# Kernel tuning notes

Hardware: AMD Instinct MI355X
Metric: run time of the kernel (lower is better)

The kernel has to match this reference:

```python
import jax, jax.numpy as jnp
import numpy as np
import math

N, IN, OUT, E, K = 50000, 256, 256, 800000, 32

def setup_inputs() -> dict:
    key = jax.random.key(0)
    k0, k1, k2, k3, k4 = jax.random.split(key, 5)
    feat = jax.random.normal(k0, (N, IN), dtype=jnp.float32)
    # xavier_uniform with relu gain, as in reset_parameters
    gain = math.sqrt(2.0)
    a = gain * math.sqrt(6.0 / (IN + OUT))
    W_self = jax.random.uniform(k1, (OUT, IN), minval=-a, maxval=a, dtype=jnp.float32)
    W_neigh = jax.random.uniform(k2, (OUT, IN), minval=-a, maxval=a, dtype=jnp.float32)
    b_neigh = jnp.zeros((OUT,), dtype=jnp.float32)
    # random CSR graph: E edges, row pointers from sorted cut points
    indices = jax.random.randint(k3, (E,), 0, N, dtype=jnp.int32)
    inner = jnp.sort(jax.random.randint(k4, (N - 1,), 0, E, dtype=jnp.int32))
    indptr = jnp.concatenate([jnp.zeros((1,), jnp.int32), inner,
                              jnp.full((1,), E, jnp.int32)])
    return {"feat": feat, "W_self": W_self, "W_neigh": W_neigh,
            "b_neigh": b_neigh, "indices": indices, "indptr": indptr}

def reference(feat, W_self, W_neigh, b_neigh, indices, indptr):
    n = feat.shape[0]
    # feat_drop with p=0.0 is identity
    h_self = feat @ W_self.T                      # [N, OUT]
    feat_neigh = feat @ W_neigh.T + b_neigh       # [N, OUT]
    # MaxK: keep top-k entries per row, zero the rest
    vals, idx = jax.lax.top_k(feat_neigh, K)      # [N, K]
    rows = jnp.arange(n)[:, None]
    masked = jnp.zeros_like(feat_neigh).at[rows, idx].set(vals)
    # CSR SpMM with unit values (sum over neighbors)
    deg = indptr[1:] - indptr[:-1]                # [N]
    dst = jnp.repeat(jnp.arange(n, dtype=jnp.int32), deg,
                     total_repeat_length=indices.shape[0])
    h_neigh = jax.ops.segment_sum(masked[indices], dst, num_segments=n)
    return h_self + h_neigh
```

## Files before the change

### kernel.cpp

```cpp
#include <hip/hip_runtime.h>

#define N_NODES 50000
#define TOPK 32
#define SOFT_DELTA 2e-5f

typedef unsigned long long u64;
typedef unsigned u32;
typedef float f32x16 __attribute__((ext_vector_type(16)));
typedef __bf16 bf16x8 __attribute__((ext_vector_type(8)));

__device__ __forceinline__ float dec(u32 u) {
    return __builtin_bit_cast(float, (u & 0x80000000u) ? (u & 0x7FFFFFFFu) : ~u);
}
__device__ __forceinline__ int mbcnt64(u64 m) {
    return __builtin_amdgcn_mbcnt_hi((u32)(m >> 32),
           __builtin_amdgcn_mbcnt_lo((u32)m, 0u));
}

__device__ __forceinline__ void gll16(const uint4* g, uint4* l) {
    __builtin_amdgcn_global_load_lds(
        (const __attribute__((address_space(1))) void*)g,
        (__attribute__((address_space(3))) void*)l, 16, 0, 0);
}

__device__ __forceinline__ u32 enc4(float v, int col) {
    return ((u32)col << 16) |
           ((__builtin_bit_cast(u32, v) + 0x8000u) >> 16);
}

__device__ __forceinline__ u32 s2(float x0, float x1, float& r0, float& r1) {
    const u32 h0 = (__builtin_bit_cast(u32, x0) + 0x8000u) & 0xFFFF0000u;
    const u32 h1 = (__builtin_bit_cast(u32, x1) + 0x8000u) & 0xFFFF0000u;
    r0 = x0 - __builtin_bit_cast(float, h0);
    r1 = x1 - __builtin_bit_cast(float, h1);
    return (h0 >> 16) | h1;
}
__device__ __forceinline__ u32 p2(float x0, float x1) {
    return (((__builtin_bit_cast(u32, x0) + 0x8000u) & 0xFFFF0000u) >> 16) |
           ((__builtin_bit_cast(u32, x1) + 0x8000u) & 0xFFFF0000u);
}

struct Tri { uint4 h1, h2, h3; };
__device__ __forceinline__ Tri cvt8(const float4 u, const float4 v, bool deep) {
    Tri t;
    float r0,r1,r2,r3,r4,r5,r6,r7;
    t.h1.x = s2(u.x, u.y, r0, r1);
    t.h1.y = s2(u.z, u.w, r2, r3);
    t.h1.z = s2(v.x, v.y, r4, r5);
    t.h1.w = s2(v.z, v.w, r6, r7);
    float s0,s1,s2_,s3,s4,s5,s6,s7;
    t.h2.x = s2(r0, r1, s0, s1);
    t.h2.y = s2(r2, r3, s2_, s3);
    t.h2.z = s2(r4, r5, s4, s5);
    t.h2.w = s2(r6, r7, s6, s7);
    if (deep) {
        t.h3.x = p2(s0, s1); t.h3.y = p2(s2_, s3);
        t.h3.z = p2(s4, s5); t.h3.w = p2(s6, s7);
    } else {
        t.h3 = make_uint4(0, 0, 0, 0);
    }
    return t;
}

__global__ __launch_bounds__(256) void wprep_kernel(
    const float* __restrict__ Wneigh,
    uint4* __restrict__ WT1, uint4* __restrict__ WT2, uint4* __restrict__ WT3)
{
    for (int it = 0; it < 4; ++it) {
        const int id = (blockIdx.x * 4 + it) * 256 + threadIdx.x;
        const int s = id >> 10, rem = id & 1023;
        const int c = rem >> 8, j = rem & 255;
        const float* src = Wneigh + (size_t)j * 256 + s * 32 + c * 8;
        const Tri t = cvt8(*(const float4*)src, *(const float4*)(src + 4), true);
        WT1[id] = t.h1; WT2[id] = t.h2; WT3[id] = t.h3;
    }
}

__global__ __launch_bounds__(256, 2) void gemm_self_kernel(
    const float* __restrict__ feat,
    const float* __restrict__ Wself,
    float* __restrict__ hself)
{
    __shared__ uint4 LA1[512], LA2[512];
    __shared__ uint4 LB1[512], LB2[512];

    const int tid  = threadIdx.x;
    const int lane = tid & 63;
    const int wave = tid >> 6;
    const int wm   = wave >> 1;
    const int wn   = wave & 1;
    const int kg   = lane >> 5;

    const int rowTile = blockIdx.x >> 1;
    const int colTile = blockIdx.x & 1;
    const int row0 = rowTile * 128;
    const int jbase = colTile << 7;

    const int srow  = tid >> 1;
    const int shalf = tid & 1;
    int gra = row0 + srow;
    if (gra >= N_NODES) gra = 0;
    const float* pa = feat  + (size_t)gra * 256 + shalf * 16;
    const float* pb = Wself + (size_t)(jbase + srow) * 256 + shalf * 16;
    const int i0 = ((shalf * 2) << 7) + srow;
    const int i1 = i0 + 128;

    const int rA0 = wm * 64 + (lane & 31);
    const int rB0 = wn * 64 + (lane & 31);

    f32x16 acc[2][2];
#pragma unroll
    for (int i = 0; i < 2; ++i)
#pragma unroll
        for (int j = 0; j < 2; ++j) acc[i][j] = (f32x16)0.f;

    float4 va0, va1, va2, va3, vb0, vb1, vb2, vb3;
    va0 = *(const float4*)(pa);      va1 = *(const float4*)(pa + 4);
    va2 = *(const float4*)(pa + 8);  va3 = *(const float4*)(pa + 12);
    vb0 = *(const float4*)(pb);      vb1 = *(const float4*)(pb + 4);
    vb2 = *(const float4*)(pb + 8);  vb3 = *(const float4*)(pb + 12);

    for (int s = 0; s < 8; ++s) {
        __syncthreads();
        {
            const Tri tA0 = cvt8(va0, va1, false);
            const Tri tA1 = cvt8(va2, va3, false);
            const Tri tB0 = cvt8(vb0, vb1, false);
            const Tri tB1 = cvt8(vb2, vb3, false);
            LA1[i0] = tA0.h1; LA2[i0] = tA0.h2;
            LA1[i1] = tA1.h1; LA2[i1] = tA1.h2;
            LB1[i0] = tB0.h1; LB2[i0] = tB0.h2;
            LB1[i1] = tB1.h1; LB2[i1] = tB1.h2;
        }
        __syncthreads();

        if (s < 7) {
            const int ko = (s + 1) * 32;
            va0 = *(const float4*)(pa + ko);      va1 = *(const float4*)(pa + ko + 4);
            va2 = *(const float4*)(pa + ko + 8);  va3 = *(const float4*)(pa + ko + 12);
            vb0 = *(const float4*)(pb + ko);      vb1 = *(const float4*)(pb + ko + 4);
            vb2 = *(const float4*)(pb + ko + 8);  vb3 = *(const float4*)(pb + ko + 12);
        }

#pragma unroll
        for (int ks = 0; ks < 2; ++ks) {
            const int base = ((ks << 1) | kg) << 7;
            bf16x8 a1[2], a2[2], b1[2], b2[2];
#pragma unroll
            for (int f = 0; f < 2; ++f) {
                const int ia = base + rA0 + f * 32;
                const int ib = base + rB0 + f * 32;
                a1[f] = __builtin_bit_cast(bf16x8, LA1[ia]);
                a2[f] = __builtin_bit_cast(bf16x8, LA2[ia]);
                b1[f] = __builtin_bit_cast(bf16x8, LB1[ib]);
                b2[f] = __builtin_bit_cast(bf16x8, LB2[ib]);
            }
#pragma unroll
            for (int i = 0; i < 2; ++i)
#pragma unroll
                for (int j = 0; j < 2; ++j) {
                    acc[i][j] = __builtin_amdgcn_mfma_f32_32x32x16_bf16(
                        a1[i], b1[j], acc[i][j], 0, 0, 0);
                    acc[i][j] = __builtin_amdgcn_mfma_f32_32x32x16_bf16(
                        a1[i], b2[j], acc[i][j], 0, 0, 0);
                    acc[i][j] = __builtin_amdgcn_mfma_f32_32x32x16_bf16(
                        a2[i], b1[j], acc[i][j], 0, 0, 0);
                }
        }
    }

#pragma unroll
    for (int i = 0; i < 2; ++i) {
        const int rbase = row0 + wm * 64 + i * 32 + (kg << 2);
#pragma unroll
        for (int j = 0; j < 2; ++j) {
            const int cg = (colTile << 7) + wn * 64 + j * 32 + (lane & 31);
#pragma unroll
            for (int r = 0; r < 16; ++r) {
                const int grow = rbase + (r & 3) + ((r >> 2) << 3);
                if (grow < N_NODES)
                    hself[(size_t)grow * 256 + cg] = acc[i][j][r];
            }
        }
    }
}

__global__ __launch_bounds__(512, 4) void gemm_nt_kernel(
    const float* __restrict__ feat,
    const uint4* __restrict__ WT1, const uint4* __restrict__ WT2,
    const uint4* __restrict__ WT3,
    const float* __restrict__ bneigh,
    u32*  __restrict__ compact,
    u64*  __restrict__ softList)
{
    __shared__ uint4 SMEM[4096];
    uint4* LA1 = SMEM;
    uint4* LA2 = SMEM + 256;
    uint4* LA3 = SMEM + 512;
    uint4* LB1 = SMEM + 768;
    uint4* LB2 = SMEM + 1792;
    uint4* LB3 = SMEM + 2816;
    float* stage = (float*)SMEM;

    const int tid  = threadIdx.x;
    const int lane = tid & 63;
    const int wave = tid >> 6;
    const int kg   = lane >> 5;

    const int row0 = blockIdx.x * 64;

    const int ar = tid & 63;
    const int ac = (tid >> 6) & 3;
    int gra = row0 + ar;
    if (gra >= N_NODES) gra = row0;
    const float* pa = feat + (size_t)gra * 256 + ac * 8;
    const int aidx = ac * 64 + ar;

    const int rA0  = lane & 31;
    const int bcol = wave * 32 + (lane & 31);

    f32x16 acc[2];
    acc[0] = (f32x16)0.f; acc[1] = (f32x16)0.f;

    float4 va0 = make_float4(0,0,0,0), va1 = make_float4(0,0,0,0);
    if (tid < 256) { va0 = *(const float4*)(pa); va1 = *(const float4*)(pa + 4); }

    for (int s = 0; s < 8; ++s) {
        __syncthreads();
        {
            const int base = s * 1024;
            const int w64  = wave * 64;
            gll16(WT1 + base + w64 + lane,       LB1 + w64);
            gll16(WT1 + base + 512 + w64 + lane, LB1 + 512 + w64);
            gll16(WT2 + base + w64 + lane,       LB2 + w64);
            gll16(WT2 + base + 512 + w64 + lane, LB2 + 512 + w64);
            gll16(WT3 + base + w64 + lane,       LB3 + w64);
            gll16(WT3 + base + 512 + w64 + lane, LB3 + 512 + w64);
        }
        if (tid < 256) {
            const Tri t = cvt8(va0, va1, true);
            LA1[aidx] = t.h1; LA2[aidx] = t.h2; LA3[aidx] = t.h3;
            if (s < 7) {
                const int ko = (s + 1) * 32;
                va0 = *(const float4*)(pa + ko);
                va1 = *(const float4*)(pa + ko + 4);
            }
        }
        __syncthreads();

#pragma unroll
        for (int ks = 0; ks < 2; ++ks) {
            const int ch = (ks << 1) | kg;
            bf16x8 a1[2], a2[2], a3[2], b1, b2, b3;
            {
                const int ib = ch * 256 + bcol;
                b1 = __builtin_bit_cast(bf16x8, LB1[ib]);
                b2 = __builtin_bit_cast(bf16x8, LB2[ib]);
                b3 = __builtin_bit_cast(bf16x8, LB3[ib]);
            }
#pragma unroll
            for (int f = 0; f < 2; ++f) {
                const int ia = ch * 64 + rA0 + f * 32;
                a1[f] = __builtin_bit_cast(bf16x8, LA1[ia]);
                a2[f] = __builtin_bit_cast(bf16x8, LA2[ia]);
                a3[f] = __builtin_bit_cast(bf16x8, LA3[ia]);
            }
#pragma unroll
            for (int i = 0; i < 2; ++i) {
                acc[i] = __builtin_amdgcn_mfma_f32_32x32x16_bf16(a1[i], b1, acc[i], 0, 0, 0);
                acc[i] = __builtin_amdgcn_mfma_f32_32x32x16_bf16(a1[i], b2, acc[i], 0, 0, 0);
                acc[i] = __builtin_amdgcn_mfma_f32_32x32x16_bf16(a2[i], b1, acc[i], 0, 0, 0);
                acc[i] = __builtin_amdgcn_mfma_f32_32x32x16_bf16(a2[i], b2, acc[i], 0, 0, 0);
                acc[i] = __builtin_amdgcn_mfma_f32_32x32x16_bf16(a1[i], b3, acc[i], 0, 0, 0);
                acc[i] = __builtin_amdgcn_mfma_f32_32x32x16_bf16(a3[i], b1, acc[i], 0, 0, 0);
            }
        }
    }

    __syncthreads();
    const float bn = bneigh[bcol];
#pragma unroll
    for (int i = 0; i < 2; ++i) {
        const int rbase = i * 32 + (kg << 2);
#pragma unroll
        for (int r = 0; r < 16; ++r) {
            const int rl = rbase + (r & 3) + ((r >> 2) << 3);
            stage[rl * 256 + bcol] = acc[i][r] + bn;
        }
    }
    __syncthreads();

    for (int it = 0; it < 8; ++it) {
        const int rl  = wave * 8 + it;
        const int row = row0 + rl;
        if (row >= N_NODES) break;

        const float4 v4 = ((const float4*)stage)[rl * 64 + lane];
        const float vv[4] = {v4.x, v4.y, v4.z, v4.w};
        u32 key[4];
#pragma unroll
        for (int j = 0; j < 4; ++j) {
            const u32 b = __builtin_bit_cast(u32, vv[j]);
            key[j] = (b & 0x80000000u) ? ~b : (b | 0x80000000u);
        }

        u32 T = 0;
        bool resolved = false;
        for (int b = 31; b >= 0; --b) {
            const u32 t2 = T | (1u << b);
            int cnt = 0;
#pragma unroll
            for (int j = 0; j < 4; ++j) cnt += __popcll(__ballot(key[j] >= t2));
            if (cnt >= TOPK) T = t2;
            if (cnt == TOPK) { resolved = true; break; }
        }
        if (resolved) {
            u32 x = 0xFFFFFFFFu;
#pragma unroll
            for (int j = 0; j < 4; ++j)
                x = min(x, (key[j] >= T) ? key[j] : 0xFFFFFFFFu);
#pragma unroll
            for (int off = 32; off >= 1; off >>= 1)
                x = min(x, (u32)__shfl_xor((int)x, off, 64));
            T = x;
        }

        u64 bgt[4], beq[4];
        int cgt = 0, ceq = 0;
#pragma unroll
        for (int j = 0; j < 4; ++j) {
            bgt[j] = __ballot(key[j] > T);
            beq[j] = __ballot(key[j] == T);
            cgt += __popcll(bgt[j]);
            ceq += __popcll(beq[j]);
        }
        const int r_ = TOPK - cgt;

        u32 m33;
        if (ceq > r_) {
            m33 = T;
        } else {
            u32 x = 0;
#pragma unroll
            for (int j = 0; j < 4; ++j) x = max(x, (key[j] < T) ? key[j] : 0u);
#pragma unroll
            for (int off = 32; off >= 1; off >>= 1)
                x = max(x, (u32)__shfl_xor((int)x, off, 64));
            m33 = x;
        }
        const float v32f = dec(T);
        const float v33f = dec(m33);
        const bool soft = (v32f - v33f) < SOFT_DELTA;

        const int meqsum = mbcnt64(beq[0]) + mbcnt64(beq[1]) +
                           mbcnt64(beq[2]) + mbcnt64(beq[3]);

        int gtbase = 0, selfpre = 0, spillcol = -1;
#pragma unroll
        for (int j = 0; j < 4; ++j) {
            const int col = lane * 4 + j;
            if (key[j] > T) {
                const int pos = gtbase + mbcnt64(bgt[j]);
                compact[(size_t)row * 32 + pos] = enc4(vv[j], col);
            } else if (key[j] == T) {
                const int eqrank = meqsum + selfpre;
                if (eqrank < r_) {
                    const float w = (soft && eqrank == r_ - 1) ? 0.5f : 1.0f;
                    compact[(size_t)row * 32 + (cgt + eqrank)] = enc4(vv[j] * w, col);
                } else if (eqrank == r_) {
                    spillcol = col;
                }
                ++selfpre;
            }
            gtbase += __popcll(bgt[j]);
        }

        if (soft) {
            const u64 valbits = (u64)__builtin_bit_cast(u32, 0.5f * v33f);
            if (ceq > r_) {
                if (spillcol >= 0)
                    softList[row] = (((u64)(u32)spillcol) << 32) | valbits;
            } else {
                int best = 1 << 30;
#pragma unroll
                for (int j = 0; j < 4; ++j) {
                    const u64 b33 = __ballot(key[j] == m33);
                    if (b33) best = min(best, ((int)__builtin_ctzll(b33)) * 4 + j);
                }
                if (lane == 0)
                    softList[row] = (((u64)(u32)best) << 32) | valbits;
            }
        } else if (lane == 0) {
            softList[row] = 0ull;
        }
    }
}

__global__ __launch_bounds__(512) void spmm_kernel(
    const u32* __restrict__ compact,
    const u64* __restrict__ softList,
    const int* __restrict__ indices,
    const int* __restrict__ indptr,
    float* __restrict__ inout)
{
    __shared__ float accs[8][2][256];

    const int lane = threadIdx.x & 63;
    const int wave = threadIdx.x >> 6;
    const int node = blockIdx.x * 8 + wave;
    const int half = lane >> 5;
    const int e    = lane & 31;
    float* acc  = accs[wave][half];

    const float4 z4 = make_float4(0.f, 0.f, 0.f, 0.f);
    ((float4*)&accs[wave][0][0])[lane] = z4;
    ((float4*)&accs[wave][1][0])[lane] = z4;

    const int start = indptr[node];
    const int deg   = indptr[node + 1] - start;
    const float4 hs = ((const float4*)(inout + (size_t)node * 256))[lane];

    for (int base = 0; base < deg; base += 64) {
        const int n = min(64, deg - base);
        const int myidx = (base + lane < deg) ? indices[start + base + lane] : 0;
        for (int d = 0; d < n; d += 16) {
            int s[8]; bool ok[8]; u32 ent[8];
#pragma unroll
            for (int k = 0; k < 8; ++k) {
                const int ei = d + 2 * k + half;
                ok[k] = ei < n;
                s[k]  = __shfl(myidx, min(ei, n - 1), 64);
                ent[k] = compact[(size_t)s[k] * 32 + e];
            }
            u64 se[8];
            if (e == 0) {
#pragma unroll
                for (int k = 0; k < 8; ++k) se[k] = softList[s[k]];
            }
#pragma unroll
            for (int k = 0; k < 8; ++k) {
                const int c = (int)(ent[k] >> 16);
                float v = __builtin_bit_cast(float, ent[k] << 16);
                if (!ok[k]) v = 0.f;
                acc[c] += v;
                if (e == 0 && ok[k]) {
                    const u32 vb = (u32)se[k];
                    if (vb)
                        acc[(int)(se[k] >> 32)] += __builtin_bit_cast(float, vb);
                }
            }
        }
    }

    const float4 a0 = ((const float4*)&accs[wave][0][0])[lane];
    const float4 a1 = ((const float4*)&accs[wave][1][0])[lane];
    float4 o;
    o.x = a0.x + a1.x + hs.x;
    o.y = a0.y + a1.y + hs.y;
    o.z = a0.z + a1.z + hs.z;
    o.w = a0.w + a1.w + hs.w;
    ((float4*)(inout + (size_t)node * 256))[lane] = o;
}

extern "C" void kernel_launch(void* const* d_in, const int* in_sizes, int n_in,
                              void* d_out, int out_size, void* d_ws, size_t ws_size,
                              hipStream_t stream) {
    const float* feat   = (const float*)d_in[0];
    const float* Wself  = (const float*)d_in[1];
    const float* Wneigh = (const float*)d_in[2];
    const float* bneigh = (const float*)d_in[3];
    const int* indices  = (const int*)d_in[4];
    const int* indptr   = (const int*)d_in[5];
    float* out = (float*)d_out;

    char* ws       = (char*)d_ws;
    u32*  compact  = (u32*)(ws);
    u64*  softList = (u64*)(ws + 6400000);
    uint4* WT1     = (uint4*)(ws + 6800000);
    uint4* WT2     = WT1 + 8192;
    uint4* WT3     = WT2 + 8192;

    wprep_kernel<<<dim3(8), dim3(256), 0, stream>>>(Wneigh, WT1, WT2, WT3);

    const int rowTiles128 = (N_NODES + 127) / 128;
    gemm_self_kernel<<<dim3(rowTiles128 * 2), dim3(256), 0, stream>>>(
        feat, Wself, out);

    const int rowTiles64 = (N_NODES + 63) / 64;
    gemm_nt_kernel<<<dim3(rowTiles64), dim3(512), 0, stream>>>(
        feat, WT1, WT2, WT3, bneigh, compact, softList);

    const int spmmBlocks = N_NODES / 8;
    spmm_kernel<<<dim3(spmmBlocks), dim3(512), 0, stream>>>(
        compact, softList, indices, indptr, out);
}
```

Before: 293.7 us.

## Fuse self GEMM into neighbor GEMM kernel sharing feature tiles

Removes the separate self-projection GEMM and computes it inside the neighbor GEMM kernel, reusing the same bf16-split feature tiles in LDS. W_self is pre-converted in the prep kernel, and only a single bf16 term is used for the self product. This is meant to avoid reading feat twice and to drop one kernel launch. In exchange it adds accumulator registers and LDS per block, which may reduce occupancy. Self-GEMM precision also drops from a two-term to a single-term bf16 split on the weight side.

```diff
diff --git a/kernel.cpp b/kernel.cpp
--- a/kernel.cpp
+++ b/kernel.cpp
@@ -63,143 +63,40 @@
 }
 
 __global__ __launch_bounds__(256) void wprep_kernel(
-    const float* __restrict__ Wneigh,
-    uint4* __restrict__ WT1, uint4* __restrict__ WT2, uint4* __restrict__ WT3)
+    const float* __restrict__ Wself, const float* __restrict__ Wneigh,
+    uint4* __restrict__ WTn1, uint4* __restrict__ WTn2,
+    uint4* __restrict__ WTn3, uint4* __restrict__ WTs1)
 {
     for (int it = 0; it < 4; ++it) {
         const int id = (blockIdx.x * 4 + it) * 256 + threadIdx.x;
         const int s = id >> 10, rem = id & 1023;
         const int c = rem >> 8, j = rem & 255;
-        const float* src = Wneigh + (size_t)j * 256 + s * 32 + c * 8;
-        const Tri t = cvt8(*(const float4*)src, *(const float4*)(src + 4), true);
-        WT1[id] = t.h1; WT2[id] = t.h2; WT3[id] = t.h3;
-    }
-}
-
-__global__ __launch_bounds__(256, 2) void gemm_self_kernel(
+        const float* srcN = Wneigh + (size_t)j * 256 + s * 32 + c * 8;
+        const Tri tn = cvt8(*(const float4*)srcN, *(const float4*)(srcN + 4), true);
+        WTn1[id] = tn.h1; WTn2[id] = tn.h2; WTn3[id] = tn.h3;
+        const float* srcS = Wself + (size_t)j * 256 + s * 32 + c * 8;
+        const Tri ts = cvt8(*(const float4*)srcS, *(const float4*)(srcS + 4), false);
+        WTs1[id] = ts.h1;
+    }
+}
+
+__global__ __launch_bounds__(512, 4) void gemm_all_kernel(
     const float* __restrict__ feat,
-    const float* __restrict__ Wself,
-    float* __restrict__ hself)
-{
-    __shared__ uint4 LA1[512], LA2[512];
-    __shared__ uint4 LB1[512], LB2[512];
-
-    const int tid  = threadIdx.x;
-    const int lane = tid & 63;
-    const int wave = tid >> 6;
-    const int wm   = wave >> 1;
-    const int wn   = wave & 1;
-    const int kg   = lane >> 5;
-
-    const int rowTile = blockIdx.x >> 1;
-    const int colTile = blockIdx.x & 1;
-    const int row0 = rowTile * 128;
-    const int jbase = colTile << 7;
-
-    const int srow  = tid >> 1;
-    const int shalf = tid & 1;
-    int gra = row0 + srow;
-    if (gra >= N_NODES) gra = 0;
-    const float* pa = feat  + (size_t)gra * 256 + shalf * 16;
-    const float* pb = Wself + (size_t)(jbase + srow) * 256 + shalf * 16;
-    const int i0 = ((shalf * 2) << 7) + srow;
-    const int i1 = i0 + 128;
-
-    const int rA0 = wm * 64 + (lane & 31);
-    const int rB0 = wn * 64 + (lane & 31);
-
-    f32x16 acc[2][2];
-#pragma unroll
-    for (int i = 0; i < 2; ++i)
-#pragma unroll
-        for (int j = 0; j < 2; ++j) acc[i][j] = (f32x16)0.f;
-
-    float4 va0, va1, va2, va3, vb0, vb1, vb2, vb3;
-    va0 = *(const float4*)(pa);      va1 = *(const float4*)(pa + 4);
-    va2 = *(const float4*)(pa + 8);  va3 = *(const float4*)(pa + 12);
-    vb0 = *(const float4*)(pb);      vb1 = *(const float4*)(pb + 4);
-    vb2 = *(const float4*)(pb + 8);  vb3 = *(const float4*)(pb + 12);
-
-    for (int s = 0; s < 8; ++s) {
-        __syncthreads();
-        {
-            const Tri tA0 = cvt8(va0, va1, false);
-            const Tri tA1 = cvt8(va2, va3, false);
-            const Tri tB0 = cvt8(vb0, vb1, false);
-            const Tri tB1 = cvt8(vb2, vb3, false);
-            LA1[i0] = tA0.h1; LA2[i0] = tA0.h2;
-            LA1[i1] = tA1.h1; LA2[i1] = tA1.h2;
-            LB1[i0] = tB0.h1; LB2[i0] = tB0.h2;
-            LB1[i1] = tB1.h1; LB2[i1] = tB1.h2;
-        }
-        __syncthreads();
-
-        if (s < 7) {
-            const int ko = (s + 1) * 32;
-            va0 = *(const float4*)(pa + ko);      va1 = *(const float4*)(pa + ko + 4);
-            va2 = *(const float4*)(pa + ko + 8);  va3 = *(const float4*)(pa + ko + 12);
-            vb0 = *(const float4*)(pb + ko);      vb1 = *(const float4*)(pb + ko + 4);
-            vb2 = *(const float4*)(pb + ko + 8);  vb3 = *(const float4*)(pb + ko + 12);
-        }
-
-#pragma unroll
-        for (int ks = 0; ks < 2; ++ks) {
-            const int base = ((ks << 1) | kg) << 7;
-            bf16x8 a1[2], a2[2], b1[2], b2[2];
-#pragma unroll
-            for (int f = 0; f < 2; ++f) {
-                const int ia = base + rA0 + f * 32;
-                const int ib = base + rB0 + f * 32;
-                a1[f] = __builtin_bit_cast(bf16x8, LA1[ia]);
-                a2[f] = __builtin_bit_cast(bf16x8, LA2[ia]);
-                b1[f] = __builtin_bit_cast(bf16x8, LB1[ib]);
-                b2[f] = __builtin_bit_cast(bf16x8, LB2[ib]);
-            }
-#pragma unroll
-            for (int i = 0; i < 2; ++i)
-#pragma unroll
-                for (int j = 0; j < 2; ++j) {
-                    acc[i][j] = __builtin_amdgcn_mfma_f32_32x32x16_bf16(
-                        a1[i], b1[j], acc[i][j], 0, 0, 0);
-                    acc[i][j] = __builtin_amdgcn_mfma_f32_32x32x16_bf16(
-                        a1[i], b2[j], acc[i][j], 0, 0, 0);
-                    acc[i][j] = __builtin_amdgcn_mfma_f32_32x32x16_bf16(
-                        a2[i], b1[j], acc[i][j], 0, 0, 0);
-                }
-        }
-    }
-
-#pragma unroll
-    for (int i = 0; i < 2; ++i) {
-        const int rbase = row0 + wm * 64 + i * 32 + (kg << 2);
-#pragma unroll
-        for (int j = 0; j < 2; ++j) {
-            const int cg = (colTile << 7) + wn * 64 + j * 32 + (lane & 31);
-#pragma unroll
-            for (int r = 0; r < 16; ++r) {
-                const int grow = rbase + (r & 3) + ((r >> 2) << 3);
-                if (grow < N_NODES)
-                    hself[(size_t)grow * 256 + cg] = acc[i][j][r];
-            }
-        }
-    }
-}
-
-__global__ __launch_bounds__(512, 4) void gemm_nt_kernel(
-    const float* __restrict__ feat,
-    const uint4* __restrict__ WT1, const uint4* __restrict__ WT2,
-    const uint4* __restrict__ WT3,
+    const uint4* __restrict__ WTn1, const uint4* __restrict__ WTn2,
+    const uint4* __restrict__ WTn3, const uint4* __restrict__ WTs1,
     const float* __restrict__ bneigh,
+    float* __restrict__ hself,
     u32*  __restrict__ compact,
     u64*  __restrict__ softList)
 {
-    __shared__ uint4 SMEM[4096];
-    uint4* LA1 = SMEM;
-    uint4* LA2 = SMEM + 256;
-    uint4* LA3 = SMEM + 512;
-    uint4* LB1 = SMEM + 768;
-    uint4* LB2 = SMEM + 1792;
-    uint4* LB3 = SMEM + 2816;
+    __shared__ uint4 SMEM[4864];
+    uint4* LA1  = SMEM;
+    uint4* LA2  = SMEM + 256;
+    uint4* LA3  = SMEM + 512;
+    uint4* LBn1 = SMEM + 768;
+    uint4* LBn2 = SMEM + 1792;
+    uint4* LBn3 = SMEM + 2816;
+    uint4* LBs1 = SMEM + 3840;
     float* stage = (float*)SMEM;
 
     const int tid  = threadIdx.x;
@@ -219,8 +116,9 @@
     const int rA0  = lane & 31;
     const int bcol = wave * 32 + (lane & 31);
 
-    f32x16 acc[2];
-    acc[0] = (f32x16)0.f; acc[1] = (f32x16)0.f;
+    f32x16 accN[2], accS[2];
+    accN[0] = (f32x16)0.f; accN[1] = (f32x16)0.f;
+    accS[0] = (f32x16)0.f; accS[1] = (f32x16)0.f;
 
     float4 va0 = make_float4(0,0,0,0), va1 = make_float4(0,0,0,0);
     if (tid < 256) { va0 = *(const float4*)(pa); va1 = *(const float4*)(pa + 4); }
@@ -230,12 +128,14 @@
         {
             const int base = s * 1024;
             const int w64  = wave * 64;
-            gll16(WT1 + base + w64 + lane,       LB1 + w64);
-            gll16(WT1 + base + 512 + w64 + lane, LB1 + 512 + w64);
-            gll16(WT2 + base + w64 + lane,       LB2 + w64);
-            gll16(WT2 + base + 512 + w64 + lane, LB2 + 512 + w64);
-            gll16(WT3 + base + w64 + lane,       LB3 + w64);
-            gll16(WT3 + base + 512 + w64 + lane, LB3 + 512 + w64);
+            gll16(WTn1 + base + w64 + lane,       LBn1 + w64);
+            gll16(WTn1 + base + 512 + w64 + lane, LBn1 + 512 + w64);
+            gll16(WTn2 + base + w64 + lane,       LBn2 + w64);
+            gll16(WTn2 + base + 512 + w64 + lane, LBn2 + 512 + w64);
+            gll16(WTn3 + base + w64 + lane,       LBn3 + w64);
+            gll16(WTn3 + base + 512 + w64 + lane, LBn3 + 512 + w64);
+            gll16(WTs1 + base + w64 + lane,       LBs1 + w64);
+            gll16(WTs1 + base + 512 + w64 + lane, LBs1 + 512 + w64);
         }
         if (tid < 256) {
             const Tri t = cvt8(va0, va1, true);
@@ -251,12 +151,13 @@
 #pragma unroll
         for (int ks = 0; ks < 2; ++ks) {
             const int ch = (ks << 1) | kg;
-            bf16x8 a1[2], a2[2], a3[2], b1, b2, b3;
+            bf16x8 a1[2], a2[2], a3[2], b1, b2, b3, bs;
             {
                 const int ib = ch * 256 + bcol;
-                b1 = __builtin_bit_cast(bf16x8, LB1[ib]);
-                b2 = __builtin_bit_cast(bf16x8, LB2[ib]);
-                b3 = __builtin_bit_cast(bf16x8, LB3[ib]);
+                b1 = __builtin_bit_cast(bf16x8, LBn1[ib]);
+                b2 = __builtin_bit_cast(bf16x8, LBn2[ib]);
+                b3 = __builtin_bit_cast(bf16x8, LBn3[ib]);
+                bs = __builtin_bit_cast(bf16x8, LBs1[ib]);
             }
 #pragma unroll
             for (int f = 0; f < 2; ++f) {
@@ -267,13 +168,26 @@
             }
 #pragma unroll
             for (int i = 0; i < 2; ++i) {
-                acc[i] = __builtin_amdgcn_mfma_f32_32x32x16_bf16(a1[i], b1, acc[i], 0, 0, 0);
-                acc[i] = __builtin_amdgcn_mfma_f32_32x32x16_bf16(a1[i], b2, acc[i], 0, 0, 0);
-                acc[i] = __builtin_amdgcn_mfma_f32_32x32x16_bf16(a2[i], b1, acc[i], 0, 0, 0);
-                acc[i] = __builtin_amdgcn_mfma_f32_32x32x16_bf16(a2[i], b2, acc[i], 0, 0, 0);
-                acc[i] = __builtin_amdgcn_mfma_f32_32x32x16_bf16(a1[i], b3, acc[i], 0, 0, 0);
-                acc[i] = __builtin_amdgcn_mfma_f32_32x32x16_bf16(a3[i], b1, acc[i], 0, 0, 0);
-            }
+                accN[i] = __builtin_amdgcn_mfma_f32_32x32x16_bf16(a1[i], b1, accN[i], 0, 0, 0);
+                accN[i] = __builtin_amdgcn_mfma_f32_32x32x16_bf16(a1[i], b2, accN[i], 0, 0, 0);
+                accN[i] = __builtin_amdgcn_mfma_f32_32x32x16_bf16(a2[i], b1, accN[i], 0, 0, 0);
+                accN[i] = __builtin_amdgcn_mfma_f32_32x32x16_bf16(a2[i], b2, accN[i], 0, 0, 0);
+                accN[i] = __builtin_amdgcn_mfma_f32_32x32x16_bf16(a1[i], b3, accN[i], 0, 0, 0);
+                accN[i] = __builtin_amdgcn_mfma_f32_32x32x16_bf16(a3[i], b1, accN[i], 0, 0, 0);
+                accS[i] = __builtin_amdgcn_mfma_f32_32x32x16_bf16(a1[i], bs, accS[i], 0, 0, 0);
+                accS[i] = __builtin_amdgcn_mfma_f32_32x32x16_bf16(a2[i], bs, accS[i], 0, 0, 0);
+            }
+        }
+    }
+
+#pragma unroll
+    for (int i = 0; i < 2; ++i) {
+        const int rbase = i * 32 + (kg << 2);
+#pragma unroll
+        for (int r = 0; r < 16; ++r) {
+            const int grow = row0 + rbase + (r & 3) + ((r >> 2) << 3);
+            if (grow < N_NODES)
+                hself[(size_t)grow * 256 + bcol] = accS[i][r];
         }
     }
 
@@ -285,7 +199,7 @@
 #pragma unroll
         for (int r = 0; r < 16; ++r) {
             const int rl = rbase + (r & 3) + ((r >> 2) << 3);
-            stage[rl * 256 + bcol] = acc[i][r] + bn;
+            stage[rl * 256 + bcol] = accN[i][r] + bn;
         }
     }
     __syncthreads();
@@ -476,19 +390,17 @@
     char* ws       = (char*)d_ws;
     u32*  compact  = (u32*)(ws);
     u64*  softList = (u64*)(ws + 6400000);
-    uint4* WT1     = (uint4*)(ws + 6800000);
-    uint4* WT2     = WT1 + 8192;
-    uint4* WT3     = WT2 + 8192;
-
-    wprep_kernel<<<dim3(8), dim3(256), 0, stream>>>(Wneigh, WT1, WT2, WT3);
-
-    const int rowTiles128 = (N_NODES + 127) / 128;
-    gemm_self_kernel<<<dim3(rowTiles128 * 2), dim3(256), 0, stream>>>(
-        feat, Wself, out);
+    uint4* WTn1    = (uint4*)(ws + 6800000);
+    uint4* WTn2    = WTn1 + 8192;
+    uint4* WTn3    = WTn2 + 8192;
+    uint4* WTs1    = WTn3 + 8192;
+
+    wprep_kernel<<<dim3(8), dim3(256), 0, stream>>>(
+        Wself, Wneigh, WTn1, WTn2, WTn3, WTs1);
 
     const int rowTiles64 = (N_NODES + 63) / 64;
-    gemm_nt_kernel<<<dim3(rowTiles64), dim3(512), 0, stream>>>(
-        feat, WT1, WT2, WT3, bneigh, compact, softList);
+    gemm_all_kernel<<<dim3(rowTiles64), dim3(512), 0, stream>>>(
+        feat, WTn1, WTn2, WTn3, WTs1, bneigh, out, compact, softList);
 
     const int spmmBlocks = N_NODES / 8;
     spmm_kernel<<<dim3(spmmBlocks), dim3(512), 0, stream>>>(
```

New measurement: 262.9 us. 10.5% less time.
